# Performance work log

Hardware: AMD Instinct MI355X
Metric: run time of the kernel (lower is better)

Reference implementation:

```python
import jax, jax.numpy as jnp
import numpy as np

B, T, D, H = 4, 2048, 1024, 16
DH = D // H


def setup_inputs() -> dict:
    key = jax.random.key(0)
    ks = jax.random.split(key, 5)
    x = jax.random.normal(ks[0], (B, T, D), dtype=jnp.float32)
    W_qkv = jax.random.normal(ks[1], (D, 3 * D), dtype=jnp.float32) * 0.02
    b_qkv = jax.random.normal(ks[2], (3 * D,), dtype=jnp.float32) * 0.02
    W_o = jax.random.normal(ks[3], (D, D), dtype=jnp.float32) * 0.02
    b_o = jax.random.normal(ks[4], (D,), dtype=jnp.float32) * 0.02
    return {"x": x, "W_qkv": W_qkv, "b_qkv": b_qkv, "W_o": W_o, "b_o": b_o}


def reference(x, W_qkv, b_qkv, W_o, b_o):
    b, t, d = x.shape
    qkv = x @ W_qkv + b_qkv                      # [b, t, 3*d]
    # 'b t (k h dh) -> k b h t dh'
    qkv = qkv.reshape(b, t, 3, H, DH).transpose(2, 0, 3, 1, 4)
    q, k, v = qkv[0], qkv[1], qkv[2]             # each [b, h, t, dh]
    scores = jnp.einsum('bhqd,bhkd->bhqk', q, k) / jnp.sqrt(jnp.float32(DH))
    causal_mask = jnp.triu(jnp.ones((t, t), dtype=bool), k=1)  # True above diag
    scores = jnp.where(causal_mask, -jnp.inf, scores)
    attn = jax.nn.softmax(scores, axis=-1)       # [b, h, t, t]
    o = jnp.einsum('bhqk,bhkd->bqhd', attn, v).reshape(b, t, d)
    return o @ W_o + b_o
```

## Files before the change

### kernel.cpp

```cpp
#include <hip/hip_runtime.h>
#include <hip/hip_bf16.h>

typedef __attribute__((ext_vector_type(8))) short bh8;
typedef __attribute__((ext_vector_type(4))) float f32x4;

#define GBL(p) (const __attribute__((address_space(1))) void*)(p)
#define LDSP(p) (__attribute__((address_space(3))) void*)(p)

__device__ __forceinline__ ushort f2bf(float f){
  union { float f; unsigned u; } v; v.f = f;
  unsigned u = v.u;
  return (ushort)((u + 0x7fffu + ((u >> 16) & 1u)) >> 16);
}

__global__ __launch_bounds__(256) void cast_x_kernel(const float4* __restrict__ in,
                                                     ushort* __restrict__ out){
  int i = blockIdx.x * 256 + threadIdx.x;
  float4 v = in[i];
  ushort4 o;
  o.x = f2bf(v.x); o.y = f2bf(v.y); o.z = f2bf(v.z); o.w = f2bf(v.w);
  *(ushort4*)&out[(size_t)i * 4] = o;
}

__global__ __launch_bounds__(256) void transpose_cast_kernel(const float* __restrict__ in,
                                                             ushort* __restrict__ out,
                                                             int R, int C){
  __shared__ float tile[32][33];
  int bx = blockIdx.x * 32;
  int by = blockIdx.y * 32;
  int tx = threadIdx.x, ty = threadIdx.y;
  #pragma unroll
  for (int i = 0; i < 32; i += 8)
    tile[ty + i][tx] = in[(size_t)(by + ty + i) * C + bx + tx];
  __syncthreads();
  #pragma unroll
  for (int i = 0; i < 32; i += 8)
    out[(size_t)(bx + ty + i) * R + by + tx] = f2bf(tile[tx][ty + i]);
}

__global__ __launch_bounds__(256) void gemm_qkv_kernel(
    const ushort* __restrict__ A,
    const ushort* __restrict__ Bt,
    const float* __restrict__ bias,
    ushort* __restrict__ Qd, ushort* __restrict__ Kd, ushort* __restrict__ Vt)
{
  constexpr int K = 1024;
  __shared__ ushort sA[8192];
  __shared__ ushort sB[8192];
  const int tid = threadIdx.x;
  const int lane = tid & 63, wave = tid >> 6;
  const int quad = lane >> 4, l16 = lane & 15;
  const int rx7 = l16 & 7;
  const int wm = (wave >> 1) * 64, wn = (wave & 1) * 64;
  const size_t aBase = (size_t)blockIdx.x * 128 * K;
  const size_t bBase = (size_t)blockIdx.y * 128 * K;
  f32x4 acc[4][4] = {};
  for (int k0 = 0; k0 < K; k0 += 64){
    #pragma unroll
    for (int c = 0; c < 4; c++){
      int u = c * 256 + tid;
      int row = u >> 3, cu = (u & 7) ^ (row & 7);
      __builtin_amdgcn_global_load_lds(GBL(A + aBase + (size_t)row * K + k0 + cu * 8),
                                       LDSP(&sA[u * 8]), 16, 0, 0);
      __builtin_amdgcn_global_load_lds(GBL(Bt + bBase + (size_t)row * K + k0 + cu * 8),
                                       LDSP(&sB[u * 8]), 16, 0, 0);
    }
    __syncthreads();
    #pragma unroll
    for (int ks = 0; ks < 2; ks++){
      bh8 af[4], bf[4];
      #pragma unroll
      for (int i = 0; i < 4; i++){
        int row = wm + i * 16 + l16;
        af[i] = *(const bh8*)&sA[row * 64 + (((ks * 4 + quad) ^ rx7) << 3)];
      }
      #pragma unroll
      for (int j = 0; j < 4; j++){
        int row = wn + j * 16 + l16;
        bf[j] = *(const bh8*)&sB[row * 64 + (((ks * 4 + quad) ^ rx7) << 3)];
      }
      #pragma unroll
      for (int i = 0; i < 4; i++)
        #pragma unroll
        for (int j = 0; j < 4; j++)
          acc[i][j] = __builtin_amdgcn_mfma_f32_16x16x32_bf16(af[i], bf[j], acc[i][j], 0, 0, 0);
    }
    __syncthreads();
  }
  const int whichBlk = (blockIdx.y * 128) >> 10;
  #pragma unroll
  for (int i = 0; i < 4; i++){
    int mg = blockIdx.x * 128 + wm + i * 16 + quad * 4;
    int bb = mg >> 11, t0 = mg & 2047;
    #pragma unroll
    for (int j = 0; j < 4; j++){
      int ng = blockIdx.y * 128 + wn + j * 16 + l16;
      float bv = bias[ng];
      int h = (ng >> 6) & 15;
      int dh = ng & 63;
      if (whichBlk == 2){
        ushort4 o;
        o.x = f2bf(acc[i][j][0] + bv);
        o.y = f2bf(acc[i][j][1] + bv);
        o.z = f2bf(acc[i][j][2] + bv);
        o.w = f2bf(acc[i][j][3] + bv);
        *(ushort4*)&Vt[((size_t)((bb * 16 + h) * 64 + dh)) * 2048 + t0] = o;
      } else {
        ushort* dst = (whichBlk == 0) ? Qd : Kd;
        float sc = (whichBlk == 0) ? 0.18033688f : 1.0f;
        #pragma unroll
        for (int r = 0; r < 4; r++)
          dst[((size_t)((bb * 16 + h) * 2048 + t0 + r) << 6) + dh] = f2bf((acc[i][j][r] + bv) * sc);
      }
    }
  }
}

__global__ __launch_bounds__(256, 4) void flash_attn_kernel(
    const ushort* __restrict__ Qd, const ushort* __restrict__ Kd,
    const ushort* __restrict__ Vt, ushort* __restrict__ Od)
{
  __shared__ ushort sK[2][4096];
  __shared__ ushort sV[2][4096];
  __shared__ ushort sP[4][1024];
  const int tid = threadIdx.x;
  const int lane = tid & 63, wave = tid >> 6;
  const int quad = lane >> 4, l16 = lane & 15;
  const int bh = blockIdx.x, pairI = blockIdx.y;
  const size_t base = (size_t)bh * (2048 * 64);
  const float SINIT = -7.2134752f;

  const int p0 = tid, p1 = 256 + tid;
  const int r0 = p0 >> 3, c0 = (p0 & 7) ^ (r0 & 7);
  const int r1 = p1 >> 3, c1 = (p1 & 7) ^ (r1 & 7);
  const ushort* kp0 = Kd + base + r0 * 64 + c0 * 8;
  const ushort* kp1 = Kd + base + r1 * 64 + c1 * 8;
  const ushort* vp0 = Vt + base + (size_t)r0 * 2048 + c0 * 8;
  const ushort* vp1 = Vt + base + (size_t)r1 * 2048 + c1 * 8;

  const int b = bh >> 4, h = bh & 15;

  #pragma unroll 1
  for (int phase = 0; phase < 2; phase++){
    const int qt = phase ? pairI : (31 - pairI);
    const ushort* qrow = Qd + base + (size_t)(qt * 64 + wave * 16 + l16) * 64 + quad * 8;
    bh8 qf0 = *(const bh8*)qrow;
    bh8 qf1 = *(const bh8*)(qrow + 32);

    f32x4 Oacc[4] = {};
    float lpart[4] = {0.f, 0.f, 0.f, 0.f};

    __syncthreads();
    __builtin_amdgcn_global_load_lds(GBL(kp0), LDSP(&sK[0][p0 * 8]), 16, 0, 0);
    __builtin_amdgcn_global_load_lds(GBL(kp1), LDSP(&sK[0][p1 * 8]), 16, 0, 0);
    __builtin_amdgcn_global_load_lds(GBL(vp0), LDSP(&sV[0][p0 * 8]), 16, 0, 0);
    __builtin_amdgcn_global_load_lds(GBL(vp1), LDSP(&sV[0][p1 * 8]), 16, 0, 0);

    #pragma unroll 1
    for (int kt = 0; kt <= qt; kt++){
      const int buf = kt & 1;
      __syncthreads();
      if (kt < qt){
        const int nb = buf ^ 1;
        __builtin_amdgcn_global_load_lds(GBL(kp0 + (kt + 1) * 4096), LDSP(&sK[nb][p0 * 8]), 16, 0, 0);
        __builtin_amdgcn_global_load_lds(GBL(kp1 + (kt + 1) * 4096), LDSP(&sK[nb][p1 * 8]), 16, 0, 0);
        __builtin_amdgcn_global_load_lds(GBL(vp0 + (kt + 1) * 64),   LDSP(&sV[nb][p0 * 8]), 16, 0, 0);
        __builtin_amdgcn_global_load_lds(GBL(vp1 + (kt + 1) * 64),   LDSP(&sV[nb][p1 * 8]), 16, 0, 0);
      }
      f32x4 S[4];
      #pragma unroll
      for (int j = 0; j < 4; j++) S[j] = (f32x4){SINIT, SINIT, SINIT, SINIT};
      #pragma unroll
      for (int ks = 0; ks < 2; ks++){
        bh8 aq = ks ? qf1 : qf0;
        #pragma unroll
        for (int j = 0; j < 4; j++){
          int row = j * 16 + l16;
          int u = row * 8 + ((ks * 4 + quad) ^ (row & 7));
          bh8 bk = *(const bh8*)&sK[buf][u * 8];
          S[j] = __builtin_amdgcn_mfma_f32_16x16x32_bf16(aq, bk, S[j], 0, 0, 0);
        }
      }
      if (kt == qt){
        #pragma unroll
        for (int j = 0; j < 4; j++)
          #pragma unroll
          for (int r = 0; r < 4; r++){
            int relq = wave * 16 + quad * 4 + r;
            int relt = j * 16 + l16;
            if (relt > relq) S[j][r] = -1e30f;
          }
      }
      #pragma unroll
      for (int j = 0; j < 4; j++){
        float pv[4];
        #pragma unroll
        for (int r = 0; r < 4; r++){
          pv[r] = exp2f(S[j][r]);
          lpart[r] += pv[r];
        }
        __hip_bfloat162 pk0 = __float22bfloat162_rn({pv[0], pv[1]});
        __hip_bfloat162 pk1 = __float22bfloat162_rn({pv[2], pv[3]});
        ushort2 w0 = *(ushort2*)&pk0, w1 = *(ushort2*)&pk1;
        ushort w[4] = {w0.x, w0.y, w1.x, w1.y};
        #pragma unroll
        for (int r = 0; r < 4; r++){
          int row = quad * 4 + r;
          int cu = 2 * j + (l16 >> 3);
          int phys = row * 8 + (cu ^ (row & 7));
          sP[wave][phys * 8 + (l16 & 7)] = w[r];
        }
      }
      #pragma unroll
      for (int ks = 0; ks < 2; ks++){
        int up = l16 * 8 + ((ks * 4 + quad) ^ (l16 & 7));
        bh8 ap = *(const bh8*)&sP[wave][up * 8];
        #pragma unroll
        for (int j = 0; j < 4; j++){
          int row = j * 16 + l16;
          int u = row * 8 + ((ks * 4 + quad) ^ (row & 7));
          bh8 bv = *(const bh8*)&sV[buf][u * 8];
          Oacc[j] = __builtin_amdgcn_mfma_f32_16x16x32_bf16(ap, bv, Oacc[j], 0, 0, 0);
        }
      }
    }
    float lr[4];
    #pragma unroll
    for (int r = 0; r < 4; r++){
      float s = lpart[r];
      s += __shfl_xor(s, 1, 64);
      s += __shfl_xor(s, 2, 64);
      s += __shfl_xor(s, 4, 64);
      s += __shfl_xor(s, 8, 64);
      lr[r] = 1.0f / s;
    }
    #pragma unroll
    for (int j = 0; j < 4; j++)
      #pragma unroll
      for (int r = 0; r < 4; r++){
        int qg = qt * 64 + wave * 16 + quad * 4 + r;
        int dh = j * 16 + l16;
        Od[(size_t)(b * 2048 + qg) * 1024 + h * 64 + dh] = f2bf(Oacc[j][r] * lr[r]);
      }
  }
}

__global__ __launch_bounds__(256) void gemm_out_kernel(
    const ushort* __restrict__ A,
    const ushort* __restrict__ Bt,
    const float* __restrict__ bias,
    float* __restrict__ out)
{
  constexpr int K = 1024;
  __shared__ ushort sA[8192];
  __shared__ ushort sB[4096];
  const int tid = threadIdx.x;
  const int lane = tid & 63, wave = tid >> 6;
  const int quad = lane >> 4, l16 = lane & 15;
  const int rx7 = l16 & 7;
  const int wm = (wave >> 1) * 64, wn = (wave & 1) * 32;
  const size_t aBase = (size_t)blockIdx.x * 128 * K;
  const size_t bBase = (size_t)blockIdx.y * 64 * K;
  f32x4 acc[4][2] = {};
  for (int k0 = 0; k0 < K; k0 += 64){
    #pragma unroll
    for (int c = 0; c < 4; c++){
      int u = c * 256 + tid;
      int row = u >> 3, cu = (u & 7) ^ (row & 7);
      __builtin_amdgcn_global_load_lds(GBL(A + aBase + (size_t)row * K + k0 + cu * 8),
                                       LDSP(&sA[u * 8]), 16, 0, 0);
    }
    #pragma unroll
    for (int c = 0; c < 2; c++){
      int u = c * 256 + tid;
      int row = u >> 3, cu = (u & 7) ^ (row & 7);
      __builtin_amdgcn_global_load_lds(GBL(Bt + bBase + (size_t)row * K + k0 + cu * 8),
                                       LDSP(&sB[u * 8]), 16, 0, 0);
    }
    __syncthreads();
    #pragma unroll
    for (int ks = 0; ks < 2; ks++){
      bh8 af[4], bf[2];
      #pragma unroll
      for (int i = 0; i < 4; i++){
        int row = wm + i * 16 + l16;
        af[i] = *(const bh8*)&sA[row * 64 + (((ks * 4 + quad) ^ rx7) << 3)];
      }
      #pragma unroll
      for (int j = 0; j < 2; j++){
        int row = wn + j * 16 + l16;
        bf[j] = *(const bh8*)&sB[row * 64 + (((ks * 4 + quad) ^ rx7) << 3)];
      }
      #pragma unroll
      for (int i = 0; i < 4; i++)
        #pragma unroll
        for (int j = 0; j < 2; j++)
          acc[i][j] = __builtin_amdgcn_mfma_f32_16x16x32_bf16(af[i], bf[j], acc[i][j], 0, 0, 0);
    }
    __syncthreads();
  }
  #pragma unroll
  for (int i = 0; i < 4; i++){
    int gm = blockIdx.x * 128 + wm + i * 16 + quad * 4;
    #pragma unroll
    for (int j = 0; j < 2; j++){
      int ng = blockIdx.y * 64 + wn + j * 16 + l16;
      float bv = bias[ng];
      #pragma unroll
      for (int r = 0; r < 4; r++)
        out[(size_t)(gm + r) * 1024 + ng] = acc[i][j][r] + bv;
    }
  }
}

extern "C" void kernel_launch(void* const* d_in, const int* in_sizes, int n_in,
                              void* d_out, int out_size, void* d_ws, size_t ws_size,
                              hipStream_t stream) {
  const float* x    = (const float*)d_in[0];
  const float* Wqkv = (const float*)d_in[1];
  const float* bqkv = (const float*)d_in[2];
  const float* Wo   = (const float*)d_in[3];
  const float* bo   = (const float*)d_in[4];
  float* out = (float*)d_out;

  char* p = (char*)d_ws;
  ushort* xb  = (ushort*)p;
  ushort* WqT = (ushort*)(p + 16777216);
  ushort* WoT = (ushort*)(p + 16777216 + 6291456);
  ushort* Qd  = (ushort*)(p + 25165824);
  ushort* Kd  = (ushort*)(p + 25165824 + 16777216);
  ushort* Vt  = (ushort*)(p + 25165824 + 33554432);
  ushort* Od  = xb;

  cast_x_kernel<<<8192, 256, 0, stream>>>((const float4*)x, xb);
  transpose_cast_kernel<<<dim3(96, 32), dim3(32, 8), 0, stream>>>(Wqkv, WqT, 1024, 3072);
  transpose_cast_kernel<<<dim3(32, 32), dim3(32, 8), 0, stream>>>(Wo, WoT, 1024, 1024);
  gemm_qkv_kernel<<<dim3(64, 24), 256, 0, stream>>>(xb, WqT, bqkv, Qd, Kd, Vt);
  flash_attn_kernel<<<dim3(64, 16), 256, 0, stream>>>(Qd, Kd, Vt, Od);
  gemm_out_kernel<<<dim3(64, 16), 256, 0, stream>>>(Od, WoT, bo, out);
}
```

Before: 259.2 us.

## Enlarge QKV GEMM tile to 256x256 with 4-stage LDS pipelined prefetch

Reworks the QKV projection GEMM to use 512-thread blocks computing 256x256 output tiles with a K-step of 32. It keeps a 4-deep ring of LDS buffers filled by direct global-to-LDS loads issued between MFMA phases, using explicit barriers, waitcnt and priority hints. The goal is to hide global load latency and raise data reuse per block. The cost is a large LDS footprint that limits blocks per CU, and a coarser grid with possible tail imbalance.

```diff
diff --git a/kernel.cpp b/kernel.cpp
--- a/kernel.cpp
+++ b/kernel.cpp
@@ -38,79 +38,126 @@
     out[(size_t)(bx + ty + i) * R + by + tx] = f2bf(tile[tx][ty + i]);
 }
 
-__global__ __launch_bounds__(256) void gemm_qkv_kernel(
+__global__ __launch_bounds__(512, 2) void gemm_qkv_kernel(
     const ushort* __restrict__ A,
     const ushort* __restrict__ Bt,
     const float* __restrict__ bias,
     ushort* __restrict__ Qd, ushort* __restrict__ Kd, ushort* __restrict__ Vt)
 {
   constexpr int K = 1024;
-  __shared__ ushort sA[8192];
-  __shared__ ushort sB[8192];
+  __shared__ ushort sA[4][8192];
+  __shared__ ushort sB[4][8192];
   const int tid = threadIdx.x;
   const int lane = tid & 63, wave = tid >> 6;
   const int quad = lane >> 4, l16 = lane & 15;
-  const int rx7 = l16 & 7;
-  const int wm = (wave >> 1) * 64, wn = (wave & 1) * 64;
-  const size_t aBase = (size_t)blockIdx.x * 128 * K;
-  const size_t bBase = (size_t)blockIdx.y * 128 * K;
-  f32x4 acc[4][4] = {};
-  for (int k0 = 0; k0 < K; k0 += 64){
-    #pragma unroll
-    for (int c = 0; c < 4; c++){
-      int u = c * 256 + tid;
-      int row = u >> 3, cu = (u & 7) ^ (row & 7);
-      __builtin_amdgcn_global_load_lds(GBL(A + aBase + (size_t)row * K + k0 + cu * 8),
-                                       LDSP(&sA[u * 8]), 16, 0, 0);
-      __builtin_amdgcn_global_load_lds(GBL(Bt + bBase + (size_t)row * K + k0 + cu * 8),
-                                       LDSP(&sB[u * 8]), 16, 0, 0);
-    }
-    __syncthreads();
-    #pragma unroll
-    for (int ks = 0; ks < 2; ks++){
-      bh8 af[4], bf[4];
-      #pragma unroll
-      for (int i = 0; i < 4; i++){
-        int row = wm + i * 16 + l16;
-        af[i] = *(const bh8*)&sA[row * 64 + (((ks * 4 + quad) ^ rx7) << 3)];
-      }
-      #pragma unroll
-      for (int j = 0; j < 4; j++){
-        int row = wn + j * 16 + l16;
-        bf[j] = *(const bh8*)&sB[row * 64 + (((ks * 4 + quad) ^ rx7) << 3)];
-      }
-      #pragma unroll
-      for (int i = 0; i < 4; i++)
-        #pragma unroll
-        for (int j = 0; j < 4; j++)
-          acc[i][j] = __builtin_amdgcn_mfma_f32_16x16x32_bf16(af[i], bf[j], acc[i][j], 0, 0, 0);
-    }
-    __syncthreads();
-  }
-  const int whichBlk = (blockIdx.y * 128) >> 10;
-  #pragma unroll
-  for (int i = 0; i < 4; i++){
-    int mg = blockIdx.x * 128 + wm + i * 16 + quad * 4;
+  const int wm = (wave >> 2) * 128, wn = (wave & 3) * 64;
+  const size_t aBase = (size_t)blockIdx.x * 256 * K;
+  const size_t bBase = (size_t)blockIdx.y * 256 * K;
+
+  const int u0 = tid, u1 = 512 + tid;
+  const int r0 = u0 >> 2, c0 = (u0 & 3) ^ ((r0 >> 1) & 3);
+  const int r1 = u1 >> 2, c1 = (u1 & 3) ^ ((r1 >> 1) & 3);
+  const ushort* a0 = A + aBase + (size_t)r0 * K + c0 * 8;
+  const ushort* a1 = A + aBase + (size_t)r1 * K + c1 * 8;
+  const ushort* b0 = Bt + bBase + (size_t)r0 * K + c0 * 8;
+  const ushort* b1 = Bt + bBase + (size_t)r1 * K + c1 * 8;
+
+  int aoff[8], boff[4];
+  #pragma unroll
+  for (int i = 0; i < 8; ++i){
+    int row = wm + i * 16 + l16;
+    aoff[i] = row * 32 + ((quad ^ ((row >> 1) & 3)) << 3);
+  }
+  #pragma unroll
+  for (int j = 0; j < 4; ++j){
+    int row = wn + j * 16 + l16;
+    boff[j] = row * 32 + ((quad ^ ((row >> 1) & 3)) << 3);
+  }
+
+  #pragma unroll
+  for (int t = 0; t < 3; ++t){
+    __builtin_amdgcn_global_load_lds(GBL(a0 + t * 32), LDSP(&sA[t][u0 * 8]), 16, 0, 0);
+    __builtin_amdgcn_global_load_lds(GBL(a1 + t * 32), LDSP(&sA[t][u1 * 8]), 16, 0, 0);
+    __builtin_amdgcn_global_load_lds(GBL(b0 + t * 32), LDSP(&sB[t][u0 * 8]), 16, 0, 0);
+    __builtin_amdgcn_global_load_lds(GBL(b1 + t * 32), LDSP(&sB[t][u1 * 8]), 16, 0, 0);
+  }
+  asm volatile("s_waitcnt vmcnt(8)" ::: "memory");
+  __builtin_amdgcn_s_barrier();
+
+  f32x4 acc[8][4] = {};
+  for (int kt = 0; kt < 32; ++kt){
+    const ushort* sa = sA[kt & 3];
+    const ushort* sb = sB[kt & 3];
+    const int ps = (kt + 3) & 3;
+    const int pf = (kt + 3 < 32) ? (kt + 3) * 32 : 31 * 32;
+
+    bh8 af0[4], bf[4];
+    #pragma unroll
+    for (int j = 0; j < 4; ++j) bf[j] = *(const bh8*)&sb[boff[j]];
+    #pragma unroll
+    for (int i = 0; i < 4; ++i) af0[i] = *(const bh8*)&sa[aoff[i]];
+    __builtin_amdgcn_global_load_lds(GBL(a0 + pf), LDSP(&sA[ps][u0 * 8]), 16, 0, 0);
+    __builtin_amdgcn_global_load_lds(GBL(a1 + pf), LDSP(&sA[ps][u1 * 8]), 16, 0, 0);
+    __builtin_amdgcn_s_barrier();
+    asm volatile("s_waitcnt lgkmcnt(0)" ::: "memory");
+    __builtin_amdgcn_sched_barrier(0);
+    __builtin_amdgcn_s_setprio(1);
+    #pragma unroll
+    for (int i = 0; i < 4; ++i)
+      #pragma unroll
+      for (int j = 0; j < 4; ++j)
+        acc[i][j] = __builtin_amdgcn_mfma_f32_16x16x32_bf16(af0[i], bf[j], acc[i][j], 0, 0, 0);
+    __builtin_amdgcn_s_setprio(0);
+    __builtin_amdgcn_s_barrier();
+
+    bh8 af1[4];
+    #pragma unroll
+    for (int i = 0; i < 4; ++i) af1[i] = *(const bh8*)&sa[aoff[4 + i]];
+    __builtin_amdgcn_global_load_lds(GBL(b0 + pf), LDSP(&sB[ps][u0 * 8]), 16, 0, 0);
+    __builtin_amdgcn_global_load_lds(GBL(b1 + pf), LDSP(&sB[ps][u1 * 8]), 16, 0, 0);
+    asm volatile("s_waitcnt vmcnt(8)" ::: "memory");
+    __builtin_amdgcn_s_barrier();
+    asm volatile("s_waitcnt lgkmcnt(0)" ::: "memory");
+    __builtin_amdgcn_sched_barrier(0);
+    __builtin_amdgcn_s_setprio(1);
+    #pragma unroll
+    for (int i = 0; i < 4; ++i)
+      #pragma unroll
+      for (int j = 0; j < 4; ++j)
+        acc[4 + i][j] = __builtin_amdgcn_mfma_f32_16x16x32_bf16(af1[i], bf[j], acc[4 + i][j], 0, 0, 0);
+    __builtin_amdgcn_s_setprio(0);
+    __builtin_amdgcn_s_barrier();
+  }
+
+  const int whichBlk = blockIdx.y >> 2;
+  float bv[4]; int ngv[4];
+  #pragma unroll
+  for (int j = 0; j < 4; ++j){
+    ngv[j] = blockIdx.y * 256 + wn + j * 16 + l16;
+    bv[j] = bias[ngv[j]];
+  }
+  #pragma unroll
+  for (int i = 0; i < 8; ++i){
+    int mg = blockIdx.x * 256 + wm + i * 16 + quad * 4;
     int bb = mg >> 11, t0 = mg & 2047;
     #pragma unroll
-    for (int j = 0; j < 4; j++){
-      int ng = blockIdx.y * 128 + wn + j * 16 + l16;
-      float bv = bias[ng];
+    for (int j = 0; j < 4; ++j){
+      int ng = ngv[j];
       int h = (ng >> 6) & 15;
       int dh = ng & 63;
       if (whichBlk == 2){
         ushort4 o;
-        o.x = f2bf(acc[i][j][0] + bv);
-        o.y = f2bf(acc[i][j][1] + bv);
-        o.z = f2bf(acc[i][j][2] + bv);
-        o.w = f2bf(acc[i][j][3] + bv);
+        o.x = f2bf(acc[i][j][0] + bv[j]);
+        o.y = f2bf(acc[i][j][1] + bv[j]);
+        o.z = f2bf(acc[i][j][2] + bv[j]);
+        o.w = f2bf(acc[i][j][3] + bv[j]);
         *(ushort4*)&Vt[((size_t)((bb * 16 + h) * 64 + dh)) * 2048 + t0] = o;
       } else {
         ushort* dst = (whichBlk == 0) ? Qd : Kd;
         float sc = (whichBlk == 0) ? 0.18033688f : 1.0f;
         #pragma unroll
         for (int r = 0; r < 4; r++)
-          dst[((size_t)((bb * 16 + h) * 2048 + t0 + r) << 6) + dh] = f2bf((acc[i][j][r] + bv) * sc);
+          dst[((size_t)((bb * 16 + h) * 2048 + t0 + r) << 6) + dh] = f2bf((acc[i][j][r] + bv[j]) * sc);
       }
     }
   }
@@ -335,7 +382,7 @@
   cast_x_kernel<<<8192, 256, 0, stream>>>((const float4*)x, xb);
   transpose_cast_kernel<<<dim3(96, 32), dim3(32, 8), 0, stream>>>(Wqkv, WqT, 1024, 3072);
   transpose_cast_kernel<<<dim3(32, 32), dim3(32, 8), 0, stream>>>(Wo, WoT, 1024, 1024);
-  gemm_qkv_kernel<<<dim3(64, 24), 256, 0, stream>>>(xb, WqT, bqkv, Qd, Kd, Vt);
+  gemm_qkv_kernel<<<dim3(32, 12), 512, 0, stream>>>(xb, WqT, bqkv, Qd, Kd, Vt);
   flash_attn_kernel<<<dim3(64, 16), 256, 0, stream>>>(Qd, Kd, Vt, Od);
   gemm_out_kernel<<<dim3(64, 16), 256, 0, stream>>>(Od, WoT, bo, out);
 }
```

New measurement: 274.2 us. 5.8% more time.
